# Kernel optimization log

Measured on AMD Instinct MI355X. Metric: run time of the kernel, lower is better.

## Reference

```python
import jax, jax.numpy as jnp
import numpy as np

RADIUS = 0.4
NSAMPLE = 32
B, N, NPOINT, C = 4, 16384, 4096, 64


def _ball_query(xyz, new_xyz, radius, nsample):
    """PointNet++ ball query: first `nsample` point indices (in original order)
    within `radius` of each query; pad with the first found index (0 if none).
    xyz: (B,N,3)  new_xyz: (B,M,3)  ->  idx: (B,M,nsample) int32."""
    n = xyz.shape[1]
    # squared distances (B, M, N) via ||a||^2 + ||b||^2 - 2 a.b
    qq = jnp.sum(new_xyz * new_xyz, axis=-1)[:, :, None]
    pp = jnp.sum(xyz * xyz, axis=-1)[:, None, :]
    d2 = qq + pp - 2.0 * jnp.einsum('bmd,bnd->bmn', new_xyz, xyz)
    ar = jnp.arange(n, dtype=jnp.int32)
    # key = point index if inside ball else sentinel n; smallest keys = earliest hits
    key = jnp.where(d2 < radius * radius, ar, n)
    neg_small, _ = jax.lax.top_k(-key, nsample)   # nsample smallest keys
    sel = -neg_small                               # (B, M, nsample)
    valid = sel < n
    first = jnp.where(valid[..., :1], sel[..., :1], 0)
    return jnp.where(valid, sel, first).astype(jnp.int32)


def setup_inputs() -> dict:
    key = jax.random.key(0)
    k1, k2, k3 = jax.random.split(key, 3)
    xyz = jax.random.normal(k1, (B, N, 3), dtype=jnp.float32)
    new_xyz = jax.random.normal(k2, (B, NPOINT, 3), dtype=jnp.float32)
    features = jax.random.normal(k3, (B, C, N), dtype=jnp.float32)
    return {"xyz": xyz, "new_xyz": new_xyz, "features": features}


def reference(xyz, new_xyz, features):
    idx = _ball_query(xyz, new_xyz, RADIUS, NSAMPLE)            # (B, M, S)
    # gather xyz -> (B, M, S, 3) -> (B, 3, M, S), center on queries
    grouped_xyz = jax.vmap(lambda p, i: p[i])(xyz, idx)
    grouped_xyz = jnp.transpose(grouped_xyz, (0, 3, 1, 2))
    grouped_xyz = grouped_xyz - jnp.transpose(new_xyz, (0, 2, 1))[..., None]
    # gather features -> (B, C, M, S)
    grouped_feat = jax.vmap(lambda f, i: f[:, i])(features, idx)
    # use_xyz=True: concat centered coords with features on channel dim
    return jnp.concatenate([grouped_xyz, grouped_feat], axis=1)  # (B, 3+C, M, S)
```

## Files before the change

### kernel.cpp

```cpp
#include <hip/hip_runtime.h>
#include <stdint.h>

#define B_ 4
#define N_ 16384
#define M_ 4096
#define C_ 64
#define S_ 32
#define R2_ 0.16f
#define GDIM 32
#define CELLS 32768
#define CSTRIDE 32772

static const size_t OFF_XYZ4  = 0;
static const size_t OFF_FT    = (size_t)B_ * N_ * 4 * sizeof(float);
static const size_t OFF_START = OFF_FT + (size_t)B_ * N_ * C_ * sizeof(float);
static const size_t OFF_CUR   = OFF_START + (size_t)B_ * CSTRIDE * sizeof(int);
static const size_t OFF_SPTS  = OFF_CUR + (size_t)B_ * CSTRIDE * sizeof(int);
static const size_t OFF_SSID  = OFF_SPTS + (size_t)B_ * N_ * 4 * sizeof(float);

__device__ __forceinline__ int cellof(float v) {
    int c = (int)floorf((v + 8.0f) * 2.0f);
    return c < 0 ? 0 : (c > GDIM - 1 ? GDIM - 1 : c);
}

__global__ __launch_bounds__(256) void pack_hist_transpose(const float* __restrict__ xyz,
                                                           float4* __restrict__ xyz4,
                                                           int* __restrict__ cur,
                                                           const float* __restrict__ f,
                                                           float* __restrict__ ft) {
    if (blockIdx.x < 256) {
        int i = blockIdx.x * 256 + threadIdx.x;
        int b = i >> 14;
        float x = __builtin_nontemporal_load(&xyz[3 * i + 0]);
        float y = __builtin_nontemporal_load(&xyz[3 * i + 1]);
        float z = __builtin_nontemporal_load(&xyz[3 * i + 2]);
        float pp = __fadd_rn(__fadd_rn(__fmul_rn(x, x), __fmul_rn(y, y)), __fmul_rn(z, z));
        xyz4[i] = make_float4(x, y, z, pp);
        int cid = (cellof(z) << 10) | (cellof(y) << 5) | cellof(x);
        atomicAdd(&cur[b * CSTRIDE + cid], 1);
    } else {
        __shared__ float tile[64][65];
        int blk = blockIdx.x - 256;
        int b  = blk >> 8;
        int n0 = (blk & 255) << 6;
        int tid  = threadIdx.x;
        int lane = tid & 63;
        int grp  = tid >> 6;
        #pragma unroll
        for (int r = 0; r < 16; ++r) {
            int c = r * 4 + grp;
            tile[c][lane] = __builtin_nontemporal_load(&f[((size_t)b * C_ + c) * N_ + n0 + lane]);
        }
        __syncthreads();
        #pragma unroll
        for (int r = 0; r < 16; ++r) {
            int nl = r * 4 + grp;
            ft[((size_t)b * N_ + n0 + nl) * C_ + lane] = tile[lane][nl];
        }
    }
}

__global__ __launch_bounds__(1024) void scan_cells(int* __restrict__ cur,
                                                   int* __restrict__ start) {
    __shared__ int ls[16];
    int b = blockIdx.x, t = threadIdx.x;
    int lane = t & 63, w = t >> 6;
    int* cb = cur + b * CSTRIDE;
    int* sb = start + b * CSTRIDE;
    int base = t * 32;
    int loc[32]; int tot = 0;
    #pragma unroll
    for (int j = 0; j < 32; ++j) { loc[j] = cb[base + j]; tot += loc[j]; }
    int pre = tot;
    #pragma unroll
    for (int o = 1; o < 64; o <<= 1) { int u = __shfl_up(pre, o); if (lane >= o) pre += u; }
    if (lane == 63) ls[w] = pre;
    __syncthreads();
    if (t < 16) {
        int v = ls[t];
        int p16 = v;
        #pragma unroll
        for (int o = 1; o < 16; o <<= 1) { int u = __shfl_up(p16, o); if (t >= o) p16 += u; }
        ls[t] = p16 - v;
    }
    __syncthreads();
    int run = ls[w] + (pre - tot);
    #pragma unroll
    for (int j = 0; j < 32; ++j) { sb[base + j] = run; cb[base + j] = run; run += loc[j]; }
    if (t == 0) sb[CELLS] = N_;
}

__global__ __launch_bounds__(256) void scatter_pts(const float4* __restrict__ xyz4,
                                                   int* __restrict__ cur,
                                                   float4* __restrict__ spts,
                                                   int* __restrict__ ssid) {
    int i = blockIdx.x * 256 + threadIdx.x;
    int b = i >> 14, n = i & (N_ - 1);
    float4 P = xyz4[i];
    int cid = (cellof(P.z) << 10) | (cellof(P.y) << 5) | cellof(P.x);
    int pos = atomicAdd(&cur[b * CSTRIDE + cid], 1);
    spts[(size_t)b * N_ + pos] = P;
    ssid[b * N_ + pos] = n;
}

__global__ __launch_bounds__(256) void bq_group(const float4* __restrict__ spts,
                                                const int* __restrict__ ssid,
                                                const int* __restrict__ start,
                                                const float* __restrict__ newxyz,
                                                const float4* __restrict__ xyz4,
                                                const float* __restrict__ ft,
                                                float* __restrict__ out) {
    __shared__ unsigned int bmAll[4][512];
    __shared__ int bcAll[4];
    int tid = threadIdx.x, lane = tid & 63, w = tid >> 6;
    unsigned int* bm = bmAll[w];
    int gw = blockIdx.x * 4 + w;
    int b = gw >> 12;
    int m = gw & (M_ - 1);

    *(uint4*)&bm[lane * 8]     = make_uint4(0u, 0u, 0u, 0u);
    *(uint4*)&bm[lane * 8 + 4] = make_uint4(0u, 0u, 0u, 0u);
    if (lane == 0) bcAll[w] = 0;

    size_t qb = ((size_t)b * M_ + m) * 3;
    float qx = newxyz[qb + 0], qy = newxyz[qb + 1], qz = newxyz[qb + 2];
    float qq = __fadd_rn(__fadd_rn(__fmul_rn(qx, qx), __fmul_rn(qy, qy)), __fmul_rn(qz, qz));
    int cx = cellof(qx), cy = cellof(qy), cz = cellof(qz);
    const float4* sp  = spts + (size_t)b * N_;
    const int*    sid = ssid + b * N_;
    const int*    st  = start + b * CSTRIDE;
    int x0 = cx > 0 ? cx - 1 : 0;
    int x1 = cx < GDIM - 1 ? cx + 1 : GDIM - 1;

    int sv = 0, ev = 0;
    if (lane < 9) {
        int dzi = lane / 3, dyi = lane - dzi * 3;
        int nz = cz + dzi - 1, ny = cy + dyi - 1;
        if ((unsigned)nz < GDIM && (unsigned)ny < GDIM) {
            float zlo = (nz == 0)        ? -1e30f : -8.0f + 0.5f * nz;
            float zhi = (nz == GDIM - 1) ?  1e30f : -8.0f + 0.5f * (nz + 1);
            float ylo = (ny == 0)        ? -1e30f : -8.0f + 0.5f * ny;
            float yhi = (ny == GDIM - 1) ?  1e30f : -8.0f + 0.5f * (ny + 1);
            float dz = fmaxf(fmaxf(zlo - qz, qz - zhi), 0.0f);
            float dy = fmaxf(fmaxf(ylo - qy, qy - yhi), 0.0f);
            float rem = R2_ + 1e-3f - dz * dz - dy * dy;
            if (rem > 0.0f) {
                float rx = sqrtf(rem) + 1e-3f;
                int xl = (int)floorf((qx - rx + 8.0f) * 2.0f);
                int xh = (int)floorf((qx + rx + 8.0f) * 2.0f);
                xl = xl < 0 ? 0 : xl;  xh = xh > GDIM - 1 ? GDIM - 1 : xh;
                xl = xl > x0 ? xl : x0;
                xh = xh < x1 ? xh : x1;
                if (xl <= xh) {
                    int rowb = (nz << 10) | (ny << 5);
                    sv = st[rowb | xl];
                    ev = st[(rowb | xh) + 1];
                }
            }
        }
    }
    __builtin_amdgcn_wave_barrier();

    #pragma unroll 1
    for (int j = 0; j < 9; ++j) {
        int s = __shfl(sv, j);
        int e = __shfl(ev, j);
        for (int i = s + lane; i < e; i += 64) {
            float4 P = sp[i];
            int o = sid[i];
            float dot = __fmaf_rn(qz, P.z, __fmaf_rn(qy, P.y, __fmul_rn(qx, P.x)));
            float d2  = __fsub_rn(__fadd_rn(qq, P.w), __fmul_rn(2.0f, dot));
            if (d2 < R2_) {
                atomicOr(&bm[o >> 5], 1u << (o & 31));
            }
        }
    }
    __builtin_amdgcn_wave_barrier();

    uint4 a = *(const uint4*)&bm[lane * 8];
    uint4 c = *(const uint4*)&bm[lane * 8 + 4];
    unsigned int wds[8] = {a.x, a.y, a.z, a.w, c.x, c.y, c.z, c.w};
    int tl = 0;
    #pragma unroll
    for (int j = 0; j < 8; ++j) tl += __popc(wds[j]);
    int pre = tl;
    #pragma unroll
    for (int o = 1; o < 64; o <<= 1) { int u = __shfl_up(pre, o); if (lane >= o) pre += u; }
    int cnt = __shfl(pre, 63);
    int r = pre - tl;
    int basei = lane << 8;
    __builtin_amdgcn_wave_barrier();
    int* sel = (int*)bm;
    #pragma unroll
    for (int wd = 0; wd < 8; ++wd) {
        if (r >= S_) break;
        unsigned int bits = wds[wd];
        while (bits && r < S_) {
            int bpos = __builtin_ctz(bits);
            bits &= bits - 1;
            int gidx = basei + (wd << 5) + bpos;
            if (r == 0) bcAll[w] = gidx;
            sel[r] = gidx;
            ++r;
        }
    }
    __builtin_amdgcn_wave_barrier();
    if (lane < S_ && lane >= cnt) sel[lane] = bcAll[w];
    __builtin_amdgcn_wave_barrier();

    int s    = lane & 31;
    int half = lane >> 5;
    int p    = sel[s];
    const float* fp = ft + (((size_t)b * N_ + p) << 6) + half * 32;
    float4 v[8];
    #pragma unroll
    for (int j = 0; j < 8; ++j) v[j] = *(const float4*)(fp + j * 4);

    const size_t cst = (size_t)M_ * S_;
    size_t ob = (((size_t)b * 67 + 3 + half * 32) * M_ + m) * S_ + s;
    #pragma unroll
    for (int j = 0; j < 8; ++j) {
        __builtin_nontemporal_store(v[j].x, &out[ob + (4 * j + 0) * cst]);
        __builtin_nontemporal_store(v[j].y, &out[ob + (4 * j + 1) * cst]);
        __builtin_nontemporal_store(v[j].z, &out[ob + (4 * j + 2) * cst]);
        __builtin_nontemporal_store(v[j].w, &out[ob + (4 * j + 3) * cst]);
    }
    if (half == 0) {
        float4 P = xyz4[(size_t)b * N_ + p];
        size_t xb = (((size_t)b * 67 + 0) * M_ + m) * S_ + s;
        __builtin_nontemporal_store(P.x - qx, &out[xb + 0 * cst]);
        __builtin_nontemporal_store(P.y - qy, &out[xb + 1 * cst]);
        __builtin_nontemporal_store(P.z - qz, &out[xb + 2 * cst]);
    }
}

extern "C" void kernel_launch(void* const* d_in, const int* in_sizes, int n_in,
                              void* d_out, int out_size, void* d_ws, size_t ws_size,
                              hipStream_t stream) {
    const float* xyz    = (const float*)d_in[0];
    const float* newxyz = (const float*)d_in[1];
    const float* feat   = (const float*)d_in[2];
    float* out = (float*)d_out;

    char* ws = (char*)d_ws;
    float4* xyz4  = (float4*)(ws + OFF_XYZ4);
    float*  ft    = (float*)(ws + OFF_FT);
    int*    startc= (int*)(ws + OFF_START);
    int*    curc  = (int*)(ws + OFF_CUR);
    float4* spts  = (float4*)(ws + OFF_SPTS);
    int*    ssid  = (int*)(ws + OFF_SSID);

    hipMemsetAsync(curc, 0, (size_t)B_ * CSTRIDE * sizeof(int), stream);
    pack_hist_transpose<<<256 + B_ * (N_ / 64), 256, 0, stream>>>(xyz, xyz4, curc, feat, ft);
    scan_cells    <<<B_, 1024, 0, stream>>>(curc, startc);
    scatter_pts   <<<(B_ * N_) / 256, 256, 0, stream>>>(xyz4, curc, spts, ssid);
    bq_group      <<<(B_ * M_) / 4, 256, 0, stream>>>(spts, ssid, startc, newxyz,
                                                      xyz4, ft, out);
}
```

Baseline: 218.1 us.

## Flatten 9 cell-row ranges into one strided loop and remap blocks per XCD

The candidate scan no longer walks the nine cell-row ranges one after another. A prefix sum over the range lengths now concatenates them into a single virtual index space that all 64 lanes stride through, with each lane mapping its index back to a memory offset through a chain of compares. This is meant to cut lane underutilisation and the per-range loop overhead when the ranges are short. Separately, blocks are remapped so that each XCD (block id mod 8) handles a single batch and nearby query indices, for better L2 locality. The cost is extra scalar setup and nine compare/selects per element.

```diff
diff --git a/kernel.cpp b/kernel.cpp
--- a/kernel.cpp
+++ b/kernel.cpp
@@ -114,9 +114,10 @@
     __shared__ int bcAll[4];
     int tid = threadIdx.x, lane = tid & 63, w = tid >> 6;
     unsigned int* bm = bmAll[w];
-    int gw = blockIdx.x * 4 + w;
-    int b = gw >> 12;
-    int m = gw & (M_ - 1);
+    int xcd = blockIdx.x & 7;
+    int b   = xcd >> 1;
+    int iw  = ((blockIdx.x >> 3) << 1) | (xcd & 1);
+    int m   = (iw << 2) | w;
 
     *(uint4*)&bm[lane * 8]     = make_uint4(0u, 0u, 0u, 0u);
     *(uint4*)&bm[lane * 8 + 4] = make_uint4(0u, 0u, 0u, 0u);
@@ -159,20 +160,46 @@
             }
         }
     }
-    __builtin_amdgcn_wave_barrier();
-
-    #pragma unroll 1
-    for (int j = 0; j < 9; ++j) {
-        int s = __shfl(sv, j);
-        int e = __shfl(ev, j);
-        for (int i = s + lane; i < e; i += 64) {
-            float4 P = sp[i];
-            int o = sid[i];
-            float dot = __fmaf_rn(qz, P.z, __fmaf_rn(qy, P.y, __fmul_rn(qx, P.x)));
-            float d2  = __fsub_rn(__fadd_rn(qq, P.w), __fmul_rn(2.0f, dot));
-            if (d2 < R2_) {
-                atomicOr(&bm[o >> 5], 1u << (o & 31));
-            }
+    int len = ev - sv;
+    int pfx = len;
+    #pragma unroll
+    for (int o = 1; o < 16; o <<= 1) { int u = __shfl_up(pfx, o); if (lane >= o) pfx += u; }
+    int L    = __builtin_amdgcn_readfirstlane(__shfl(pfx, 8));
+    int badj = sv - (pfx - len);
+    int sb0 = __builtin_amdgcn_readfirstlane(__shfl(badj, 0));
+    int sb1 = __builtin_amdgcn_readfirstlane(__shfl(badj, 1));
+    int sb2 = __builtin_amdgcn_readfirstlane(__shfl(badj, 2));
+    int sb3 = __builtin_amdgcn_readfirstlane(__shfl(badj, 3));
+    int sb4 = __builtin_amdgcn_readfirstlane(__shfl(badj, 4));
+    int sb5 = __builtin_amdgcn_readfirstlane(__shfl(badj, 5));
+    int sb6 = __builtin_amdgcn_readfirstlane(__shfl(badj, 6));
+    int sb7 = __builtin_amdgcn_readfirstlane(__shfl(badj, 7));
+    int sb8 = __builtin_amdgcn_readfirstlane(__shfl(badj, 8));
+    int se1 = __builtin_amdgcn_readfirstlane(__shfl(pfx, 0));
+    int se2 = __builtin_amdgcn_readfirstlane(__shfl(pfx, 1));
+    int se3 = __builtin_amdgcn_readfirstlane(__shfl(pfx, 2));
+    int se4 = __builtin_amdgcn_readfirstlane(__shfl(pfx, 3));
+    int se5 = __builtin_amdgcn_readfirstlane(__shfl(pfx, 4));
+    int se6 = __builtin_amdgcn_readfirstlane(__shfl(pfx, 5));
+    int se7 = __builtin_amdgcn_readfirstlane(__shfl(pfx, 6));
+    int se8 = __builtin_amdgcn_readfirstlane(__shfl(pfx, 7));
+
+    for (int t = lane; t < L; t += 64) {
+        int off = sb0 + t;
+        if (t >= se1) off = sb1 + t;
+        if (t >= se2) off = sb2 + t;
+        if (t >= se3) off = sb3 + t;
+        if (t >= se4) off = sb4 + t;
+        if (t >= se5) off = sb5 + t;
+        if (t >= se6) off = sb6 + t;
+        if (t >= se7) off = sb7 + t;
+        if (t >= se8) off = sb8 + t;
+        float4 P = sp[off];
+        int o = sid[off];
+        float dot = __fmaf_rn(qz, P.z, __fmaf_rn(qy, P.y, __fmul_rn(qx, P.x)));
+        float d2  = __fsub_rn(__fadd_rn(qq, P.w), __fmul_rn(2.0f, dot));
+        if (d2 < R2_) {
+            atomicOr(&bm[o >> 5], 1u << (o & 31));
         }
     }
     __builtin_amdgcn_wave_barrier();
```

After: 216.6 us. About the same (-0.7%).
